# Optimization experiments

Measured on AMD Instinct MI355X. Metric: run time of the kernel, lower is better.

Reference implementation:

```python
import jax, jax.numpy as jnp
import numpy as np

D_MODEL = 1024
NUM_HEADS = 16
SEQ = 2048
BATCH = 4


def setup_inputs() -> dict:
    key = jax.random.key(0)
    ks = jax.random.split(key, 9)
    d = D_MODEL
    s = 0.02
    return {
        "x": jax.random.normal(ks[0], (BATCH, SEQ, d), dtype=jnp.float32),
        "WQ_w": jax.random.normal(ks[1], (d, d), dtype=jnp.float32) * s,
        "WQ_b": jnp.zeros((d,), dtype=jnp.float32),
        "WK_w": jax.random.normal(ks[2], (d, d), dtype=jnp.float32) * s,
        "WK_b": jnp.zeros((d,), dtype=jnp.float32),
        "WV_w": jax.random.normal(ks[3], (d, d), dtype=jnp.float32) * s,
        "WV_b": jnp.zeros((d,), dtype=jnp.float32),
        "WO_w": jax.random.normal(ks[4], (d, d), dtype=jnp.float32) * s,
        "WO_b": jnp.zeros((d,), dtype=jnp.float32),
    }


def reference(x, WQ_w, WQ_b, WK_w, WK_b, WV_w, WV_b, WO_w, WO_b):
    b, s, d = x.shape
    n = NUM_HEADS
    dk = d // n
    # projections (torch nn.Linear: y = x @ W.T + b)
    Q = x @ WQ_w.T + WQ_b
    K = x @ WK_w.T + WK_b
    V = x @ WV_w.T + WV_b
    # [b, s, n*dk] -> [b, n, s, dk]
    Q = Q.reshape(b, s, n, dk).transpose(0, 2, 1, 3)
    K = K.reshape(b, s, n, dk).transpose(0, 2, 1, 3)
    V = V.reshape(b, s, n, dk).transpose(0, 2, 1, 3)
    scale = 1.0 / jnp.sqrt(jnp.asarray(dk, dtype=Q.dtype))
    scores = jnp.einsum('bnqd,bnkd->bnqk', Q, K) * scale  # [b,n,s,s]
    causal = jnp.tril(jnp.ones((s, s), dtype=bool))
    scores = jnp.where(causal[None, None], scores, -jnp.inf)
    attn = jax.nn.softmax(scores, axis=-1)
    out = jnp.einsum('bnqk,bnkd->bnqd', attn, V)  # [b,n,s,dk]
    out = out.transpose(0, 2, 1, 3).reshape(b, s, d)  # merge heads
    return out @ WO_w.T + WO_b
```

## Files before the change

kernel.cpp:

```cpp
#include <hip/hip_runtime.h>
#include <hip/hip_bf16.h>
#include <stdint.h>

#define D_MODEL 1024
#define NHEAD 16
#define SEQ 2048
#define BATCH 4
#define DK 64
#define QKVSTR 3072

typedef __attribute__((ext_vector_type(8))) short short8;
typedef __attribute__((ext_vector_type(4))) float f32x4;
typedef __attribute__((ext_vector_type(16))) float f32x16;

#if __has_builtin(__builtin_amdgcn_exp2f)
#define EXP2(x) __builtin_amdgcn_exp2f(x)
#else
#define EXP2(x) exp2f(x)
#endif

__device__ inline unsigned short f2bf(float f) {
  unsigned int u = __builtin_bit_cast(unsigned int, f);
  unsigned int r = (u + 0x7fffu + ((u >> 16) & 1u)) >> 16;
  return (unsigned short)r;
}

__device__ inline unsigned int cvt_pk_bf16(float lo, float hi) {
  unsigned int d;
  asm("v_cvt_pk_bf16_f32 %0, %1, %2" : "=v"(d) : "v"(lo), "v"(hi));
  return d;
}

#define GLOAD_LDS16(g, l) \
  __builtin_amdgcn_global_load_lds((const __attribute__((address_space(1))) unsigned int*)(g), \
      (__attribute__((address_space(3))) unsigned int*)(l), 16, 0, 0)

__global__ void cvt_kernel(const float* __restrict__ in, unsigned short* __restrict__ out, int n) {
  int i = (blockIdx.x * 256 + threadIdx.x) * 8;
  if (i >= n) return;
  const float4* p = (const float4*)(in + i);
  float4 a = p[0], b = p[1];
  union { unsigned short u[8]; uint4 v; } r;
  r.u[0] = f2bf(a.x); r.u[1] = f2bf(a.y); r.u[2] = f2bf(a.z); r.u[3] = f2bf(a.w);
  r.u[4] = f2bf(b.x); r.u[5] = f2bf(b.y); r.u[6] = f2bf(b.z); r.u[7] = f2bf(b.w);
  *(uint4*)(out + i) = r.v;
}

__global__ void cvt4_kernel(const float* __restrict__ i0, const float* __restrict__ i1,
                            const float* __restrict__ i2, const float* __restrict__ i3,
                            unsigned short* __restrict__ out, int n) {
  const int by = blockIdx.y;
  const float* in = (by == 0) ? i0 : (by == 1) ? i1 : (by == 2) ? i2 : i3;
  unsigned short* o = out + (size_t)by * n;
  int i = (blockIdx.x * 256 + threadIdx.x) * 8;
  if (i >= n) return;
  const float4* p = (const float4*)(in + i);
  float4 a = p[0], b = p[1];
  union { unsigned short u[8]; uint4 v; } r;
  r.u[0] = f2bf(a.x); r.u[1] = f2bf(a.y); r.u[2] = f2bf(a.z); r.u[3] = f2bf(a.w);
  r.u[4] = f2bf(b.x); r.u[5] = f2bf(b.y); r.u[6] = f2bf(b.z); r.u[7] = f2bf(b.w);
  *(uint4*)(o + i) = r.v;
}

template <typename CT>
__global__ __launch_bounds__(256)
void gemm_bt(const unsigned short* __restrict__ A, const unsigned short* __restrict__ B,
             const float* __restrict__ b0, const float* __restrict__ b1,
             const float* __restrict__ b2, CT* __restrict__ C, int M, int N, int K,
             int qcols, float alphaQ) {
  __shared__ unsigned short As[128 * 64];
  __shared__ unsigned short Bs[128 * 64];
  const int t = threadIdx.x;
  const int l = t & 63;
  const int w = t >> 6;
  const int wr = w >> 1, wc = w & 1;
  const int l15 = l & 15, lg = l >> 4;
  const int m0 = blockIdx.y * 128, n0 = blockIdx.x * 128;

  f32x4 acc[4][4] = {};

  const int srow = t >> 3;
  const int sc8 = t & 7;
  const int kssw = sc8 ^ (srow & 7);

  const unsigned short* ap = A + (size_t)(m0 + srow) * K + kssw * 8;
  const unsigned short* bp = B + (size_t)(n0 + srow) * K + kssw * 8;

  const int nt = K >> 6;
  for (int kt = 0; kt < nt; ++kt) {
    const int k0 = kt * 64;
    #pragma unroll
    for (int j = 0; j < 4; ++j) {
      GLOAD_LDS16(ap + (size_t)(j * 32) * K + k0, &As[(j * 32 + srow) * 64 + sc8 * 8]);
      GLOAD_LDS16(bp + (size_t)(j * 32) * K + k0, &Bs[(j * 32 + srow) * 64 + sc8 * 8]);
    }
    asm volatile("s_waitcnt vmcnt(0)" ::: "memory");
    __builtin_amdgcn_s_barrier();
    __builtin_amdgcn_sched_barrier(0);

    __builtin_amdgcn_s_setprio(1);
    #pragma unroll
    for (int kk = 0; kk < 2; ++kk) {
      short8 af[4], bfr[4];
      #pragma unroll
      for (int m = 0; m < 4; ++m) {
        int row = wr * 64 + m * 16 + l15;
        af[m] = *(const short8*)&As[row * 64 + (((kk * 4 + lg) ^ (row & 7)) * 8)];
      }
      #pragma unroll
      for (int n = 0; n < 4; ++n) {
        int row = wc * 64 + n * 16 + l15;
        bfr[n] = *(const short8*)&Bs[row * 64 + (((kk * 4 + lg) ^ (row & 7)) * 8)];
      }
      #pragma unroll
      for (int m = 0; m < 4; ++m)
        #pragma unroll
        for (int n = 0; n < 4; ++n)
          acc[m][n] = __builtin_amdgcn_mfma_f32_16x16x32_bf16(af[m], bfr[n], acc[m][n], 0, 0, 0);
    }
    __builtin_amdgcn_s_setprio(0);

    __builtin_amdgcn_s_barrier();
    __builtin_amdgcn_sched_barrier(0);
  }

  #pragma unroll
  for (int m = 0; m < 4; ++m) {
    #pragma unroll
    for (int n = 0; n < 4; ++n) {
      int col = n0 + wc * 64 + n * 16 + l15;
      const float* bp2 = (col < 1024) ? b0 : (col < 2048) ? b1 : b2;
      float bz = bp2[col & 1023];
      #pragma unroll
      for (int r = 0; r < 4; ++r) {
        int row = m0 + wr * 64 + m * 16 + lg * 4 + r;
        float v = acc[m][n][r] + bz;
        if (col < qcols) v *= alphaQ;
        if constexpr (sizeof(CT) == 2) {
          C[(size_t)row * N + col] = (CT)f2bf(v);
        } else {
          C[(size_t)row * N + col] = v;
        }
      }
    }
  }
}

__global__ __launch_bounds__(256, 2)
void attn_kernel(const unsigned short* __restrict__ QKV, unsigned short* __restrict__ AO) {
  __shared__ unsigned short Ks[2][64 * 64];
  __shared__ unsigned int Vt32[64 * 33];

  const int t = threadIdx.x;
  const int l = t & 63;
  const int wave = t >> 6;
  const int l31 = l & 31, lh = l >> 5;
  const int id = blockIdx.x;
  const int qb = 15 - (id >> 6);
  const int bh = id & 63;
  const int b = bh >> 4, h = bh & 15;
  const size_t hbase = (size_t)b * SEQ * QKVSTR + h * DK;
  const size_t hbaseO = (size_t)b * SEQ * D_MODEL + h * DK;

  const int q = qb * 128 + wave * 32 + l31;

  short8 qf[4];
  {
    const unsigned short* qp = QKV + hbase + (size_t)q * QKVSTR + lh * 8;
    qf[0] = *(const short8*)(qp);
    qf[1] = *(const short8*)(qp + 16);
    qf[2] = *(const short8*)(qp + 32);
    qf[3] = *(const short8*)(qp + 48);
  }

  f32x16 o0 = {}, o1 = {};
  float lacc = 0.f;

  const int srow = t >> 3, sc8 = t & 7;
  const int kssw = sc8 ^ (srow & 7);
  const int vp_ = t & 31;
  const int vdh = (t >> 5) * 8;
  const int vpos = (vp_ & 0x19) | ((vp_ & 2) << 1) | ((vp_ & 4) >> 1);

  auto issueK = [&](int kvt, int buf) {
    const unsigned short* kp = QKV + hbase + 1024 + (size_t)(kvt * 64 + srow) * QKVSTR + kssw * 8;
    GLOAD_LDS16(kp, &Ks[buf][srow * 64 + sc8 * 8]);
    GLOAD_LDS16(kp + (size_t)32 * QKVSTR, &Ks[buf][(32 + srow) * 64 + sc8 * 8]);
  };

  const int ntiles = 2 * qb + 2;

  short8 cv0, cv1;
  issueK(0, 0);
  {
    const unsigned short* vp = QKV + hbase + 2048 + (size_t)(2 * vp_) * QKVSTR + vdh;
    cv0 = *(const short8*)vp;
    cv1 = *(const short8*)(vp + QKVSTR);
  }

  int p = 0;
  for (int kvt = 0; kvt < ntiles; ++kvt) {
    const int kv0 = kvt * 64;
    asm volatile("s_waitcnt vmcnt(0)" ::: "memory");
    __builtin_amdgcn_s_barrier();
    __builtin_amdgcn_sched_barrier(0);

    #pragma unroll
    for (int j = 0; j < 8; ++j) {
      unsigned int dw = (unsigned int)(unsigned short)cv0[j] |
                        ((unsigned int)(unsigned short)cv1[j] << 16);
      Vt32[(vdh + j) * 33 + vpos] = dw;
    }
    short8 nv0 = cv0, nv1 = cv1;
    if (kvt + 1 < ntiles) {
      issueK(kvt + 1, p ^ 1);
      const unsigned short* vp = QKV + hbase + 2048 + (size_t)(kv0 + 64 + 2 * vp_) * QKVSTR + vdh;
      nv0 = *(const short8*)vp;
      nv1 = *(const short8*)(vp + QKVSTR);
    }
    asm volatile("s_waitcnt lgkmcnt(0)" ::: "memory");
    __builtin_amdgcn_s_barrier();
    __builtin_amdgcn_sched_barrier(0);

    f32x16 s0 = {}, s1 = {};
    __builtin_amdgcn_s_setprio(1);
    #pragma unroll
    for (int kg = 0; kg < 4; ++kg) {
      int row0 = l31;
      int row1 = 32 + l31;
      int c = 2 * kg + lh;
      short8 kf0 = *(const short8*)&Ks[p][row0 * 64 + ((c ^ (row0 & 7)) * 8)];
      short8 kf1 = *(const short8*)&Ks[p][row1 * 64 + ((c ^ (row1 & 7)) * 8)];
      s0 = __builtin_amdgcn_mfma_f32_32x32x16_bf16(kf0, qf[kg], s0, 0, 0, 0);
      s1 = __builtin_amdgcn_mfma_f32_32x32x16_bf16(kf1, qf[kg], s1, 0, 0, 0);
    }
    __builtin_amdgcn_s_setprio(0);

    if (kvt >= ntiles - 2) {
      #pragma unroll
      for (int g = 0; g < 4; ++g)
        #pragma unroll
        for (int e = 0; e < 4; ++e) {
          int kvl = 8 * g + e + 4 * lh;
          if (kv0 + kvl > q)      s0[4 * g + e] = -INFINITY;
          if (kv0 + 32 + kvl > q) s1[4 * g + e] = -INFINITY;
        }
    }

    {
      float ps0 = 0.f, ps1 = 0.f, ps2 = 0.f, ps3 = 0.f;
      #pragma unroll
      for (int i = 0; i < 4; ++i) {
        s0[i]      = EXP2(s0[i]);      ps0 += s0[i];
        s0[i + 4]  = EXP2(s0[i + 4]);  ps1 += s0[i + 4];
        s0[i + 8]  = EXP2(s0[i + 8]);  ps2 += s0[i + 8];
        s0[i + 12] = EXP2(s0[i + 12]); ps3 += s0[i + 12];
      }
      #pragma unroll
      for (int i = 0; i < 4; ++i) {
        s1[i]      = EXP2(s1[i]);      ps0 += s1[i];
        s1[i + 4]  = EXP2(s1[i + 4]);  ps1 += s1[i + 4];
        s1[i + 8]  = EXP2(s1[i + 8]);  ps2 += s1[i + 8];
        s1[i + 12] = EXP2(s1[i + 12]); ps3 += s1[i + 12];
      }
      lacc += (ps0 + ps1) + (ps2 + ps3);
    }

    __builtin_amdgcn_s_setprio(1);
    #pragma unroll
    for (int win = 0; win < 4; ++win) {
      const int base = 8 * (win & 1);
      uint4 pu;
      if (win < 2) {
        pu.x = cvt_pk_bf16(s0[base + 0], s0[base + 1]);
        pu.y = cvt_pk_bf16(s0[base + 2], s0[base + 3]);
        pu.z = cvt_pk_bf16(s0[base + 4], s0[base + 5]);
        pu.w = cvt_pk_bf16(s0[base + 6], s0[base + 7]);
      } else {
        pu.x = cvt_pk_bf16(s1[base + 0], s1[base + 1]);
        pu.y = cvt_pk_bf16(s1[base + 2], s1[base + 3]);
        pu.z = cvt_pk_bf16(s1[base + 4], s1[base + 5]);
        pu.w = cvt_pk_bf16(s1[base + 6], s1[base + 7]);
      }
      short8 pb = __builtin_bit_cast(short8, pu);
      uint4 u0 = *(const uint4*)&Vt32[(l31) * 33 + win * 8 + lh * 4];
      uint4 u1 = *(const uint4*)&Vt32[(32 + l31) * 33 + win * 8 + lh * 4];
      o0 = __builtin_amdgcn_mfma_f32_32x32x16_bf16(__builtin_bit_cast(short8, u0), pb, o0, 0, 0, 0);
      o1 = __builtin_amdgcn_mfma_f32_32x32x16_bf16(__builtin_bit_cast(short8, u1), pb, o1, 0, 0, 0);
    }
    __builtin_amdgcn_s_setprio(0);

    cv0 = nv0; cv1 = nv1;
    p ^= 1;
  }

  lacc += __shfl_xor(lacc, 32, 64);
  float inv = 1.f / lacc;
  unsigned short* op = AO + hbaseO + (size_t)q * D_MODEL;
  #pragma unroll
  for (int g = 0; g < 4; ++g) {
    int d0 = 8 * g + 4 * lh;
    ushort4 v0, v1;
    v0.x = f2bf(o0[4 * g + 0] * inv); v0.y = f2bf(o0[4 * g + 1] * inv);
    v0.z = f2bf(o0[4 * g + 2] * inv); v0.w = f2bf(o0[4 * g + 3] * inv);
    v1.x = f2bf(o1[4 * g + 0] * inv); v1.y = f2bf(o1[4 * g + 1] * inv);
    v1.z = f2bf(o1[4 * g + 2] * inv); v1.w = f2bf(o1[4 * g + 3] * inv);
    *(ushort4*)(op + d0) = v0;
    *(ushort4*)(op + 32 + d0) = v1;
  }
}

extern "C" void kernel_launch(void* const* d_in, const int* in_sizes, int n_in,
                              void* d_out, int out_size, void* d_ws, size_t ws_size,
                              hipStream_t stream) {
  const float* x   = (const float*)d_in[0];
  const float* WQw = (const float*)d_in[1];
  const float* WQb = (const float*)d_in[2];
  const float* WKw = (const float*)d_in[3];
  const float* WKb = (const float*)d_in[4];
  const float* WVw = (const float*)d_in[5];
  const float* WVb = (const float*)d_in[6];
  const float* WOw = (const float*)d_in[7];
  const float* WOb = (const float*)d_in[8];
  float* out = (float*)d_out;

  const int M = BATCH * SEQ;
  const int D = D_MODEL;
  const int NX = M * D;
  const int NW = D * D;

  unsigned short* xb = (unsigned short*)d_ws;
  unsigned short* wq = xb + NX;
  unsigned short* wo = wq + 3 * NW;
  unsigned short* QKVb = wq + 4 * NW;
  unsigned short* AOb = xb;

  cvt_kernel<<<NX / 8 / 256, 256, 0, stream>>>(x, xb, NX);
  cvt4_kernel<<<dim3(NW / 8 / 256, 4), 256, 0, stream>>>(WQw, WKw, WVw, WOw, wq, NW);

  const float qscale = 0.125f * 1.4426950408889634f;
  gemm_bt<unsigned short><<<dim3(3 * D / 128, M / 128), 256, 0, stream>>>(
      xb, wq, WQb, WKb, WVb, QKVb, M, 3 * D, D, 1024, qscale);

  attn_kernel<<<1024, 256, 0, stream>>>(QKVb, AOb);

  gemm_bt<float><<<dim3(D / 128, M / 128), 256, 0, stream>>>(
      AOb, wo, WOb, WOb, WOb, out, M, D, D, 0, 1.0f);
}
```

Baseline: 150.7 us.

## Split KV range for long causal query blocks and merge partials

For the eight longest query blocks (qb 8..15), the attention work is split across two workgroups, each covering half of the KV tiles. Each half writes unnormalised fp32 partial outputs and row sums to workspace, and a new combine kernel adds them and normalises to bf16. The aim is better load balance and a shorter tail in causal attention, where later query blocks do far more work. The cost is an extra kernel launch, roughly 33 MB of fp32 partial traffic, and a dependence on the workspace being large enough; otherwise the old single-pass path runs.

```diff
diff --git a/kernel.cpp b/kernel.cpp
--- a/kernel.cpp
+++ b/kernel.cpp
@@ -147,7 +147,8 @@
 }
 
 __global__ __launch_bounds__(256, 2)
-void attn_kernel(const unsigned short* __restrict__ QKV, unsigned short* __restrict__ AO) {
+void attn_kernel(const unsigned short* __restrict__ QKV, unsigned short* __restrict__ AO,
+                 float* __restrict__ po, float* __restrict__ pl, int mode) {
   __shared__ unsigned short Ks[2][64 * 64];
   __shared__ unsigned int Vt32[64 * 33];
 
@@ -156,13 +157,32 @@
   const int wave = t >> 6;
   const int l31 = l & 31, lh = l >> 5;
   const int id = blockIdx.x;
-  const int qb = 15 - (id >> 6);
   const int bh = id & 63;
   const int b = bh >> 4, h = bh & 15;
+
+  int qb, kvA, kvB, half = -1, slot = 0;
+  if (mode) {
+    const int j = id >> 6;
+    if (j < 16) {
+      qb = 15 - (j >> 1);
+      half = j & 1;
+      slot = (j >> 1) * 64 + bh;
+      const int mid = qb + 1;
+      kvA = half ? mid : 0;
+      kvB = half ? 2 * qb + 2 : mid;
+    } else {
+      qb = 23 - j;
+      kvA = 0; kvB = 2 * qb + 2;
+    }
+  } else {
+    qb = 15 - (id >> 6);
+    kvA = 0; kvB = 2 * qb + 2;
+  }
+
   const size_t hbase = (size_t)b * SEQ * QKVSTR + h * DK;
   const size_t hbaseO = (size_t)b * SEQ * D_MODEL + h * DK;
-
-  const int q = qb * 128 + wave * 32 + l31;
+  const int qloc = wave * 32 + l31;
+  const int q = qb * 128 + qloc;
 
   short8 qf[4];
   {
@@ -188,18 +208,16 @@
     GLOAD_LDS16(kp + (size_t)32 * QKVSTR, &Ks[buf][(32 + srow) * 64 + sc8 * 8]);
   };
 
-  const int ntiles = 2 * qb + 2;
-
   short8 cv0, cv1;
-  issueK(0, 0);
+  issueK(kvA, 0);
   {
-    const unsigned short* vp = QKV + hbase + 2048 + (size_t)(2 * vp_) * QKVSTR + vdh;
+    const unsigned short* vp = QKV + hbase + 2048 + (size_t)(kvA * 64 + 2 * vp_) * QKVSTR + vdh;
     cv0 = *(const short8*)vp;
     cv1 = *(const short8*)(vp + QKVSTR);
   }
 
   int p = 0;
-  for (int kvt = 0; kvt < ntiles; ++kvt) {
+  for (int kvt = kvA; kvt < kvB; ++kvt) {
     const int kv0 = kvt * 64;
     asm volatile("s_waitcnt vmcnt(0)" ::: "memory");
     __builtin_amdgcn_s_barrier();
@@ -212,7 +230,7 @@
       Vt32[(vdh + j) * 33 + vpos] = dw;
     }
     short8 nv0 = cv0, nv1 = cv1;
-    if (kvt + 1 < ntiles) {
+    if (kvt + 1 < kvB) {
       issueK(kvt + 1, p ^ 1);
       const unsigned short* vp = QKV + hbase + 2048 + (size_t)(kv0 + 64 + 2 * vp_) * QKVSTR + vdh;
       nv0 = *(const short8*)vp;
@@ -236,7 +254,7 @@
     }
     __builtin_amdgcn_s_setprio(0);
 
-    if (kvt >= ntiles - 2) {
+    if (kvt >= 2 * qb) {
       #pragma unroll
       for (int g = 0; g < 4; ++g)
         #pragma unroll
@@ -295,19 +313,57 @@
   }
 
   lacc += __shfl_xor(lacc, 32, 64);
-  float inv = 1.f / lacc;
-  unsigned short* op = AO + hbaseO + (size_t)q * D_MODEL;
-  #pragma unroll
-  for (int g = 0; g < 4; ++g) {
-    int d0 = 8 * g + 4 * lh;
-    ushort4 v0, v1;
-    v0.x = f2bf(o0[4 * g + 0] * inv); v0.y = f2bf(o0[4 * g + 1] * inv);
-    v0.z = f2bf(o0[4 * g + 2] * inv); v0.w = f2bf(o0[4 * g + 3] * inv);
-    v1.x = f2bf(o1[4 * g + 0] * inv); v1.y = f2bf(o1[4 * g + 1] * inv);
-    v1.z = f2bf(o1[4 * g + 2] * inv); v1.w = f2bf(o1[4 * g + 3] * inv);
-    *(ushort4*)(op + d0) = v0;
-    *(ushort4*)(op + 32 + d0) = v1;
-  }
+
+  if (half >= 0) {
+    float* myo = po + ((size_t)(slot * 2 + half) * 128 + qloc) * 64;
+    #pragma unroll
+    for (int g = 0; g < 4; ++g) {
+      int d0 = 8 * g + 4 * lh;
+      float4 f0 = make_float4(o0[4 * g + 0], o0[4 * g + 1], o0[4 * g + 2], o0[4 * g + 3]);
+      float4 f1 = make_float4(o1[4 * g + 0], o1[4 * g + 1], o1[4 * g + 2], o1[4 * g + 3]);
+      *(float4*)(myo + d0) = f0;
+      *(float4*)(myo + 32 + d0) = f1;
+    }
+    if (lh == 0) pl[(size_t)(slot * 2 + half) * 128 + qloc] = lacc;
+  } else {
+    float inv = 1.f / lacc;
+    unsigned short* op = AO + hbaseO + (size_t)q * D_MODEL;
+    #pragma unroll
+    for (int g = 0; g < 4; ++g) {
+      int d0 = 8 * g + 4 * lh;
+      ushort4 v0, v1;
+      v0.x = f2bf(o0[4 * g + 0] * inv); v0.y = f2bf(o0[4 * g + 1] * inv);
+      v0.z = f2bf(o0[4 * g + 2] * inv); v0.w = f2bf(o0[4 * g + 3] * inv);
+      v1.x = f2bf(o1[4 * g + 0] * inv); v1.y = f2bf(o1[4 * g + 1] * inv);
+      v1.z = f2bf(o1[4 * g + 2] * inv); v1.w = f2bf(o1[4 * g + 3] * inv);
+      *(ushort4*)(op + d0) = v0;
+      *(ushort4*)(op + 32 + d0) = v1;
+    }
+  }
+}
+
+__global__ __launch_bounds__(256)
+void combine_kernel(const float* __restrict__ po, const float* __restrict__ pl,
+                    unsigned short* __restrict__ AO) {
+  const int idx = blockIdx.x * 256 + threadIdx.x;
+  const int row = idx >> 4;
+  const int dch = (idx & 15) * 4;
+  const int slot = row >> 7, qloc = row & 127;
+  const float4 a = *(const float4*)(po + ((size_t)(slot * 2) * 128 + qloc) * 64 + dch);
+  const float4 c = *(const float4*)(po + ((size_t)(slot * 2 + 1) * 128 + qloc) * 64 + dch);
+  const float lsum = pl[(size_t)(slot * 2) * 128 + qloc] + pl[(size_t)(slot * 2 + 1) * 128 + qloc];
+  const float inv = 1.f / lsum;
+  const int s7 = slot >> 6, bh = slot & 63;
+  const int qb = 15 - s7;
+  const int q = qb * 128 + qloc;
+  const int b = bh >> 4, h = bh & 15;
+  unsigned short* op = AO + (size_t)b * SEQ * D_MODEL + (size_t)q * D_MODEL + h * DK + dch;
+  ushort4 v;
+  v.x = f2bf((a.x + c.x) * inv);
+  v.y = f2bf((a.y + c.y) * inv);
+  v.z = f2bf((a.z + c.z) * inv);
+  v.w = f2bf((a.w + c.w) * inv);
+  *(ushort4*)op = v;
 }
 
 extern "C" void kernel_launch(void* const* d_in, const int* in_sizes, int n_in,
@@ -335,6 +391,11 @@
   unsigned short* QKVb = wq + 4 * NW;
   unsigned short* AOb = xb;
 
+  float* po = (float*)(QKVb + (size_t)M * 3072);
+  float* pl = po + (size_t)512 * 2 * 128 * 64;
+  const size_t need = (size_t)((char*)(pl + 512 * 2 * 128) - (char*)d_ws);
+  const int split = (ws_size >= need) ? 1 : 0;
+
   cvt_kernel<<<NX / 8 / 256, 256, 0, stream>>>(x, xb, NX);
   cvt4_kernel<<<dim3(NW / 8 / 256, 4), 256, 0, stream>>>(WQw, WKw, WVw, WOw, wq, NW);
 
@@ -342,7 +403,12 @@
   gemm_bt<unsigned short><<<dim3(3 * D / 128, M / 128), 256, 0, stream>>>(
       xb, wq, WQb, WKb, WVb, QKVb, M, 3 * D, D, 1024, qscale);
 
-  attn_kernel<<<1024, 256, 0, stream>>>(QKVb, AOb);
+  if (split) {
+    attn_kernel<<<1536, 256, 0, stream>>>(QKVb, AOb, po, pl, 1);
+    combine_kernel<<<4096, 256, 0, stream>>>(po, pl, AOb);
+  } else {
+    attn_kernel<<<1024, 256, 0, stream>>>(QKVb, AOb, po, pl, 0);
+  }
 
   gemm_bt<float><<<dim3(D / 128, M / 128), 256, 0, stream>>>(
       AOb, wo, WOb, WOb, WOb, out, M, D, D, 0, 1.0f);
```

Result: slower. 161.7 us (+7.3%).
